# Performance work log

Measured on AMD Instinct MI355X. Metric: run time of the kernel, lower is better.

Reference implementation:

```python
import math
import jax, jax.numpy as jnp
import numpy as np

CAPACITY_FACTOR = 1.25
TOP_K = 2
LN_EPS = 1e-5


def setup_inputs() -> dict:
    key = jax.random.key(0)
    ks = jax.random.split(key, 4)
    B, S, D, F, E = 8, 4096, 256, 512, 8
    x = jax.random.normal(ks[0], (B, S, D), dtype=jnp.float32)
    Wr = jax.random.normal(ks[1], (D, E), dtype=jnp.float32) / np.sqrt(D)
    br = jnp.zeros((E,), jnp.float32)
    W1 = jax.random.normal(ks[2], (E, D, F), dtype=jnp.float32) / np.sqrt(D)
    b1 = jnp.zeros((E, F), jnp.float32)
    W2 = jax.random.normal(ks[3], (E, F, D), dtype=jnp.float32) / np.sqrt(F)
    b2 = jnp.zeros((E, D), jnp.float32)
    gamma = jnp.ones((D,), jnp.float32)
    beta = jnp.zeros((D,), jnp.float32)
    return {"x": x, "Wr": Wr, "br": br, "W1": W1, "b1": b1,
            "W2": W2, "b2": b2, "gamma": gamma, "beta": beta}


def _layer_norm(x, gamma, beta):
    mu = jnp.mean(x, axis=-1, keepdims=True)
    var = jnp.var(x, axis=-1, keepdims=True)
    return (x - mu) * jax.lax.rsqrt(var + LN_EPS) * gamma + beta


def reference(x, Wr, br, W1, b1, W2, b2, gamma, beta):
    B, S, D = x.shape
    E = Wr.shape[1]
    N = B * S
    K = TOP_K

    # --- Router: per-sequence softmax routing weights [B, E] ---
    logits = jnp.mean(x, axis=1) @ Wr + br              # [B, E]
    routing_weights = jax.nn.softmax(logits, axis=-1)   # [B, E]

    # --- Capacity constraints (SparseMoELayer._apply_capacity_constraints) ---
    capacity = float(math.ceil(N * CAPACITY_FACTOR / E))
    expected_loads = routing_weights.sum(axis=0) * (N / B)          # [E]
    scale = jnp.where(expected_loads > capacity,
                      capacity / expected_loads, 1.0)               # [E]
    routing_weights = jax.nn.softmax(routing_weights * scale, axis=-1)

    # --- Expand to tokens and take top-k, renormalize with softmax ---
    rw_tok = jnp.broadcast_to(routing_weights[:, None, :], (B, S, E)).reshape(N, E)
    top_w, top_i = jax.lax.top_k(rw_tok, K)             # [N, K]
    top_w = jax.nn.softmax(top_w, axis=-1)

    # --- Expert FFNs (dense compute over all experts, sparse combine) ---
    xf = x.reshape(N, D)
    h = jax.nn.gelu(jnp.einsum('nd,edf->enf', xf, W1) + b1[:, None, :],
                    approximate=False)                  # [E, N, F]
    y = jnp.einsum('enf,efd->end', h, W2) + b2[:, None, :]  # [E, N, D]

    # dense combine weights [N, E] via scatter-add of top-k weights
    w_dense = jnp.zeros((N, E), x.dtype).at[jnp.arange(N)[:, None], top_i].add(top_w)
    out = jnp.einsum('ne,end->nd', w_dense, y).reshape(B, S, D)

    # residual + layer norm
    out = _layer_norm(out + x, gamma, beta)
    return out
```

## Files before the change

### kernel.cpp

```cpp
#include <hip/hip_runtime.h>
#include <math.h>


#define B_ 8
#define S_ 4096
#define D_ 256
#define F_ 512
#define E_ 8

typedef short bf16x8 __attribute__((ext_vector_type(8)));
typedef float f32x4 __attribute__((ext_vector_type(4)));

static __device__ __forceinline__ unsigned short f2bf(float f) {
    union { float f; unsigned int i; } v; v.f = f;
    unsigned int x = v.i;
    return (unsigned short)((x + 0x7fffu + ((x >> 16) & 1u)) >> 16);
}

static __device__ __forceinline__ unsigned int cvt_pk_bf16(float s0, float s1) {
    unsigned int r;
    asm("v_cvt_pk_bf16_f32 %0, %1, %2" : "=v"(r) : "v"(s0), "v"(s1));
    return r;
}

static __device__ __forceinline__ void bar_lds() {
    asm volatile("s_waitcnt lgkmcnt(0)" ::: "memory");
    __builtin_amdgcn_s_barrier();
}

static __device__ __forceinline__ float gelu_f(float v) {
    float x = fabsf(v) * 0.70710678118654752f;
    float t = __builtin_amdgcn_rcpf(1.0f + 0.3275911f * x);
    float p = t * (0.254829592f +
              t * (-0.284496736f +
              t * (1.421413741f +
              t * (-1.453152027f +
              t * 1.061405429f))));
    float er = 1.0f - p * __expf(-x * x);
    er = __builtin_copysignf(er, v);
    return 0.5f * v * (1.0f + er);
}

__global__ void k_prep(const float* __restrict__ x,
                       double* __restrict__ partial,
                       const float* __restrict__ W1,
                       const float* __restrict__ W2,
                       unsigned short* __restrict__ W1T,
                       unsigned short* __restrict__ W2T) {
    int bid = blockIdx.x;
    if (bid < 512) {
        int b = bid >> 6;
        int c = bid & 63;
        int d = threadIdx.x;
        const float* p = x + ((size_t)(b * S_ + c * 64) * D_ + d);
        double acc = 0.0;
        #pragma unroll 8
        for (int i = 0; i < 64; ++i) acc += (double)p[(size_t)i * D_];
        partial[(size_t)bid * D_ + d] = acc;
        return;
    }
    __shared__ float tile[32][33];
    const float* src;
    unsigned short* dst;
    int R, C, cb, rb;
    if (bid < 1536) {
        int b2 = bid - 512;
        int e = b2 >> 7, rem = b2 & 127;
        int by = rem >> 4, bx = rem & 15;
        R = 256; C = 512;
        src = W1 + (size_t)e * R * C;
        dst = W1T + (size_t)e * R * C;
        cb = bx * 32; rb = by * 32;
    } else {
        int b2 = bid - 1536;
        int e = b2 >> 7, rem = b2 & 127;
        int by = rem >> 3, bx = rem & 7;
        R = 512; C = 256;
        src = W2 + (size_t)e * R * C;
        dst = W2T + (size_t)e * R * C;
        cb = bx * 32; rb = by * 32;
    }
    int tx = threadIdx.x & 31, ty = threadIdx.x >> 5;
    #pragma unroll
    for (int k = 0; k < 4; ++k)
        tile[ty + 8 * k][tx] = src[(size_t)(rb + ty + 8 * k) * C + cb + tx];
    __syncthreads();
    #pragma unroll
    for (int k = 0; k < 4; ++k)
        dst[(size_t)(cb + ty + 8 * k) * R + rb + tx] = f2bf(tile[tx][ty + 8 * k]);
}

__global__ void k_red2(const double* __restrict__ partial,
                       const float* __restrict__ Wr,
                       const float* __restrict__ br,
                       double* __restrict__ lgout) {
    __shared__ double xs[256];
    int bb = blockIdx.x;
    int t = threadIdx.x;
    double acc = 0.0;
    #pragma unroll 8
    for (int c = 0; c < 64; ++c)
        acc += partial[(size_t)(bb * 64 + c) * D_ + t];
    xs[t] = acc;
    __syncthreads();
    if (t < 8) {
        int e = t;
        double a2 = 0.0;
        for (int d = 0; d < D_; ++d)
            a2 += (xs[d] * (1.0 / (double)S_)) * (double)Wr[d * E_ + e];
        lgout[bb * 8 + e] = a2 + (double)br[e];
    }
}

__global__ void k_router(const double* __restrict__ lgin,
                         float* __restrict__ route) {
    __shared__ double lg[64];
    __shared__ double rw[8][8];
    int t = threadIdx.x;
    if (t < 64) lg[t] = lgin[t];
    __syncthreads();
    if (t < 8) {
        int bb = t;
        double m = -1e300;
        for (int ee = 0; ee < 8; ++ee) m = fmax(m, lg[bb * 8 + ee]);
        double s = 0.0;
        double p[8];
        for (int ee = 0; ee < 8; ++ee) { p[ee] = exp(lg[bb * 8 + ee] - m); s += p[ee]; }
        for (int ee = 0; ee < 8; ++ee) rw[bb][ee] = p[ee] / s;
    }
    __syncthreads();
    if (t < 8) {
        int bb = t;
        const double capacity = 5120.0;
        double scale[8];
        for (int ee = 0; ee < 8; ++ee) {
            double load = 0.0;
            for (int b2 = 0; b2 < 8; ++b2) load += rw[b2][ee];
            load *= 4096.0;
            scale[ee] = load > capacity ? capacity / load : 1.0;
        }
        double v[8];
        double m = -1e300;
        for (int ee = 0; ee < 8; ++ee) { v[ee] = rw[bb][ee] * scale[ee]; m = fmax(m, v[ee]); }
        double s = 0.0;
        for (int ee = 0; ee < 8; ++ee) { v[ee] = exp(v[ee] - m); s += v[ee]; }
        for (int ee = 0; ee < 8; ++ee) v[ee] /= s;
        int i1 = 0;
        for (int ee = 1; ee < 8; ++ee) if (v[ee] > v[i1]) i1 = ee;
        int i2 = (i1 == 0) ? 1 : 0;
        for (int ee = 0; ee < 8; ++ee) { if (ee == i1) continue; if (v[ee] > v[i2]) i2 = ee; }
        double d21 = v[i2] - v[i1];
        double ed = exp(d21);
        double w1 = 1.0 / (1.0 + ed);
        double w2 = ed * w1;
        route[bb * 4 + 0] = (float)i1;
        route[bb * 4 + 1] = (float)i2;
        route[bb * 4 + 2] = (float)w1;
        route[bb * 4 + 3] = (float)w2;
    }
}

__launch_bounds__(512, 4)
__global__ void k_moe_m(const float* __restrict__ xf,
                        const unsigned short* __restrict__ W1T,
                        const unsigned short* __restrict__ W2T,
                        const float* __restrict__ b1,
                        const float* __restrict__ b2,
                        const float* __restrict__ gamma,
                        const float* __restrict__ beta,
                        const float* __restrict__ route,
                        float* __restrict__ out) {
    __shared__ __align__(16) unsigned short Xsb[64][264];
    __shared__ __align__(16) unsigned short Hsb[2][64][136];
    __shared__ float gbuf[256], bbuf[256];
    __shared__ __align__(16) float rred[64][20];

    const int t = threadIdx.x;
    const int wv = t >> 6;
    const int lane = t & 63;
    const int g = lane >> 4;
    const int c = lane & 15;
    const int b = blockIdx.x & 7;
    const int m0 = (blockIdx.x >> 3) * 64;

    if (t < 256) { gbuf[t] = gamma[t]; bbuf[t] = beta[t]; }

    const int e0i = (int)route[b * 4 + 0];
    const int e1i = (int)route[b * 4 + 1];
    const float rw0 = route[b * 4 + 2];
    const float rw1 = route[b * 4 + 3];

    {
        int row = t >> 3;
        int col0 = (t & 7) * 32;
        const float* src = xf + ((size_t)(b * S_ + m0 + row) * D_ + col0);
        #pragma unroll
        for (int jg = 0; jg < 4; ++jg) {
            float4 a0 = *(const float4*)(src + jg * 8);
            float4 a1 = *(const float4*)(src + jg * 8 + 4);
            union { unsigned int pk[4]; uint4 q; } o;
            o.pk[0] = cvt_pk_bf16(a0.x, a0.y);
            o.pk[1] = cvt_pk_bf16(a0.z, a0.w);
            o.pk[2] = cvt_pk_bf16(a1.x, a1.y);
            o.pk[3] = cvt_pk_bf16(a1.z, a1.w);
            *(uint4*)&Xsb[row][col0 + jg * 8] = o.q;
        }
    }

    f32x4 Yacc[4][2];
    #pragma unroll
    for (int i = 0; i < 4; ++i)
        #pragma unroll
        for (int j = 0; j < 2; ++j)
            #pragma unroll
            for (int r = 0; r < 4; ++r) Yacc[i][j][r] = 0.f;

    bf16x8 w1f[8];
    {
        const unsigned short* w1p0 =
            W1T + ((size_t)(e0i * F_ + wv * 16 + c)) * D_ + g * 8;
        #pragma unroll
        for (int kc = 0; kc < 8; ++kc)
            w1f[kc] = *(const bf16x8*)(w1p0 + kc * 32);
    }

    bar_lds();

    int pb = 0;
    for (int it = 0; it < 8; ++it) {
        const int sl = it >> 2;
        const int fb = it & 3;
        const int e = sl ? e1i : e0i;
        const float w = sl ? rw1 : rw0;

        const unsigned short* w2p =
            W2T + ((size_t)(e * D_ + wv * 32 + c)) * F_ + fb * 128 + g * 8;
        bf16x8 w2f[4][2];
        #pragma unroll
        for (int kc = 0; kc < 4; ++kc)
            #pragma unroll
            for (int nt = 0; nt < 2; ++nt)
                w2f[kc][nt] = *(const bf16x8*)(w2p + (size_t)(nt * 16) * F_ + kc * 32);

        float4 bias4 = *(const float4*)&b1[e * F_ + fb * 128 + wv * 16 + g * 4];

        f32x4 Hacc[4];
        #pragma unroll
        for (int i = 0; i < 4; ++i)
            #pragma unroll
            for (int r = 0; r < 4; ++r) Hacc[i][r] = 0.f;
        #pragma unroll
        for (int kc = 0; kc < 8; ++kc) {
            #pragma unroll
            for (int mt = 0; mt < 4; ++mt) {
                bf16x8 a = *(const bf16x8*)&Xsb[mt * 16 + c][kc * 32 + g * 8];
                Hacc[mt] = __builtin_amdgcn_mfma_f32_16x16x32_bf16(w1f[kc], a, Hacc[mt], 0, 0, 0);
            }
        }

        #pragma unroll
        for (int mt = 0; mt < 4; ++mt) {
            float h0 = w * gelu_f(Hacc[mt][0] + bias4.x);
            float h1 = w * gelu_f(Hacc[mt][1] + bias4.y);
            float h2 = w * gelu_f(Hacc[mt][2] + bias4.z);
            float h3 = w * gelu_f(Hacc[mt][3] + bias4.w);
            uint2 q;
            q.x = cvt_pk_bf16(h0, h1);
            q.y = cvt_pk_bf16(h2, h3);
            *(uint2*)&Hsb[pb][mt * 16 + c][wv * 16 + g * 4] = q;
        }

        {
            const int itn = (it + 1) & 7;
            const int en = (itn >> 2) ? e1i : e0i;
            const int fbn = itn & 3;
            const unsigned short* w1pn =
                W1T + ((size_t)(en * F_ + fbn * 128 + wv * 16 + c)) * D_ + g * 8;
            #pragma unroll
            for (int kc = 0; kc < 8; ++kc)
                w1f[kc] = *(const bf16x8*)(w1pn + kc * 32);
        }

        bar_lds();

        #pragma unroll
        for (int kc = 0; kc < 4; ++kc) {
            #pragma unroll
            for (int mt = 0; mt < 4; ++mt) {
                bf16x8 a = *(const bf16x8*)&Hsb[pb][mt * 16 + c][kc * 32 + g * 8];
                #pragma unroll
                for (int nt = 0; nt < 2; ++nt)
                    Yacc[mt][nt] = __builtin_amdgcn_mfma_f32_16x16x32_bf16(a, w2f[kc][nt], Yacc[mt][nt], 0, 0, 0);
            }
        }
        pb ^= 1;
    }

    float bias2[2];
    #pragma unroll
    for (int nt = 0; nt < 2; ++nt) {
        int d = wv * 32 + nt * 16 + c;
        bias2[nt] = rw0 * b2[e0i * D_ + d] + rw1 * b2[e1i * D_ + d];
    }
    #pragma unroll
    for (int mt = 0; mt < 4; ++mt)
        #pragma unroll
        for (int r = 0; r < 4; ++r) {
            int row = mt * 16 + g * 4 + r;
            const float* xr = xf + (size_t)(b * S_ + m0 + row) * D_;
            float s = 0.f, sq = 0.f;
            #pragma unroll
            for (int nt = 0; nt < 2; ++nt) {
                int d = wv * 32 + nt * 16 + c;
                float v = Yacc[mt][nt][r] + bias2[nt] + xr[d];
                Yacc[mt][nt][r] = v;
                s += v; sq += v * v;
            }
            s += __shfl_xor(s, 1); sq += __shfl_xor(sq, 1);
            s += __shfl_xor(s, 2); sq += __shfl_xor(sq, 2);
            s += __shfl_xor(s, 4); sq += __shfl_xor(sq, 4);
            s += __shfl_xor(s, 8); sq += __shfl_xor(sq, 8);
            if (c == 0) { rred[row][wv * 2] = s; rred[row][wv * 2 + 1] = sq; }
        }
    bar_lds();
    #pragma unroll
    for (int mt = 0; mt < 4; ++mt)
        #pragma unroll
        for (int r = 0; r < 4; ++r) {
            int row = mt * 16 + g * 4 + r;
            float4 p0 = *(const float4*)&rred[row][0];
            float4 p1 = *(const float4*)&rred[row][4];
            float4 p2 = *(const float4*)&rred[row][8];
            float4 p3 = *(const float4*)&rred[row][12];
            float s  = ((p0.x + p1.x) + (p2.x + p3.x)) + ((p0.z + p1.z) + (p2.z + p3.z));
            float sq = ((p0.y + p1.y) + (p2.y + p3.y)) + ((p0.w + p1.w) + (p2.w + p3.w));
            float mu = s * (1.0f / 256.0f);
            float var = sq * (1.0f / 256.0f) - mu * mu;
            float rstd = rsqrtf(var + 1e-5f);
            float* op = out + (size_t)(b * S_ + m0 + row) * D_;
            #pragma unroll
            for (int nt = 0; nt < 2; ++nt) {
                int d = wv * 32 + nt * 16 + c;
                op[d] = (Yacc[mt][nt][r] - mu) * rstd * gbuf[d] + bbuf[d];
            }
        }
}

extern "C" void kernel_launch(void* const* d_in, const int* in_sizes, int n_in,
                              void* d_out, int out_size, void* d_ws, size_t ws_size,
                              hipStream_t stream) {
    const float* x     = (const float*)d_in[0];
    const float* Wr    = (const float*)d_in[1];
    const float* br    = (const float*)d_in[2];
    const float* W1    = (const float*)d_in[3];
    const float* b1    = (const float*)d_in[4];
    const float* W2    = (const float*)d_in[5];
    const float* b2    = (const float*)d_in[6];
    const float* gamma = (const float*)d_in[7];
    const float* beta  = (const float*)d_in[8];
    float* out = (float*)d_out;

    char* ws = (char*)d_ws;
    double* partial = (double*)ws;
    float* route  = (float*)(ws + 1064960);
    double* lg    = (double*)(ws + 1065472);
    unsigned short* W1T = (unsigned short*)(ws + 1081344);
    unsigned short* W2T = (unsigned short*)(ws + 3178496);

    hipLaunchKernelGGL(k_prep, dim3(2560), dim3(256), 0, stream,
                       x, partial, W1, W2, W1T, W2T);
    hipLaunchKernelGGL(k_red2, dim3(8), dim3(256), 0, stream,
                       partial, Wr, br, lg);
    hipLaunchKernelGGL(k_router, dim3(1), dim3(64), 0, stream,
                       lg, route);
    hipLaunchKernelGGL(k_moe_m, dim3(512), dim3(512), 0, stream,
                       x, W1T, W2T, b1, b2, gamma, beta, route, out);
}
```

Before: 201.9 us.

## Software-pipeline expert FFN loop so GEMM2 of previous block overlaps GELU

Restructures the 8-step expert loop into a prologue, a skewed steady state and an epilogue. Each iteration now computes GEMM1 for block it, then interleaves the GELU/pack of those results with the GEMM2 MFMAs of block it-1 read from the other LDS buffer. This leaves one barrier per iteration and overlaps transcendental VALU work with matrix work. The cost is a more complex control flow, a longer-lived w2f register set and possible register pressure.

```diff
diff --git a/kernel.cpp b/kernel.cpp
--- a/kernel.cpp
+++ b/kernel.cpp
@@ -226,24 +226,10 @@
 
     bar_lds();
 
-    int pb = 0;
-    for (int it = 0; it < 8; ++it) {
-        const int sl = it >> 2;
-        const int fb = it & 3;
-        const int e = sl ? e1i : e0i;
-        const float w = sl ? rw1 : rw0;
-
-        const unsigned short* w2p =
-            W2T + ((size_t)(e * D_ + wv * 32 + c)) * F_ + fb * 128 + g * 8;
-        bf16x8 w2f[4][2];
-        #pragma unroll
-        for (int kc = 0; kc < 4; ++kc)
-            #pragma unroll
-            for (int nt = 0; nt < 2; ++nt)
-                w2f[kc][nt] = *(const bf16x8*)(w2p + (size_t)(nt * 16) * F_ + kc * 32);
-
-        float4 bias4 = *(const float4*)&b1[e * F_ + fb * 128 + wv * 16 + g * 4];
-
+    bf16x8 w2f[4][2];
+
+    {
+        float4 bias4 = *(const float4*)&b1[e0i * F_ + wv * 16 + g * 4];
         f32x4 Hacc[4];
         #pragma unroll
         for (int i = 0; i < 4; ++i)
@@ -257,43 +243,109 @@
                 Hacc[mt] = __builtin_amdgcn_mfma_f32_16x16x32_bf16(w1f[kc], a, Hacc[mt], 0, 0, 0);
             }
         }
-
         #pragma unroll
         for (int mt = 0; mt < 4; ++mt) {
-            float h0 = w * gelu_f(Hacc[mt][0] + bias4.x);
-            float h1 = w * gelu_f(Hacc[mt][1] + bias4.y);
-            float h2 = w * gelu_f(Hacc[mt][2] + bias4.z);
-            float h3 = w * gelu_f(Hacc[mt][3] + bias4.w);
+            float h0 = rw0 * gelu_f(Hacc[mt][0] + bias4.x);
+            float h1 = rw0 * gelu_f(Hacc[mt][1] + bias4.y);
+            float h2 = rw0 * gelu_f(Hacc[mt][2] + bias4.z);
+            float h3 = rw0 * gelu_f(Hacc[mt][3] + bias4.w);
             uint2 q;
             q.x = cvt_pk_bf16(h0, h1);
             q.y = cvt_pk_bf16(h2, h3);
-            *(uint2*)&Hsb[pb][mt * 16 + c][wv * 16 + g * 4] = q;
-        }
-
-        {
-            const int itn = (it + 1) & 7;
-            const int en = (itn >> 2) ? e1i : e0i;
+            *(uint2*)&Hsb[0][mt * 16 + c][wv * 16 + g * 4] = q;
+        }
+        const unsigned short* w1pn =
+            W1T + ((size_t)(e0i * F_ + 128 + wv * 16 + c)) * D_ + g * 8;
+        #pragma unroll
+        for (int kc = 0; kc < 8; ++kc)
+            w1f[kc] = *(const bf16x8*)(w1pn + kc * 32);
+        bar_lds();
+    }
+
+    for (int it = 1; it < 8; ++it) {
+        const int e  = (it >= 4) ? e1i : e0i;
+        const float w = (it >= 4) ? rw1 : rw0;
+        const int fb = it & 3;
+        const int ep  = ((it - 1) >= 4) ? e1i : e0i;
+        const int fbp = (it - 1) & 3;
+        const int wb = it & 1;
+
+        const unsigned short* w2p =
+            W2T + ((size_t)(ep * D_ + wv * 32 + c)) * F_ + fbp * 128 + g * 8;
+        #pragma unroll
+        for (int kc = 0; kc < 4; ++kc)
+            #pragma unroll
+            for (int nt = 0; nt < 2; ++nt)
+                w2f[kc][nt] = *(const bf16x8*)(w2p + (size_t)(nt * 16) * F_ + kc * 32);
+
+        float4 bias4 = *(const float4*)&b1[e * F_ + fb * 128 + wv * 16 + g * 4];
+
+        f32x4 Hacc[4];
+        #pragma unroll
+        for (int i = 0; i < 4; ++i)
+            #pragma unroll
+            for (int r = 0; r < 4; ++r) Hacc[i][r] = 0.f;
+        #pragma unroll
+        for (int kc = 0; kc < 8; ++kc) {
+            #pragma unroll
+            for (int mt = 0; mt < 4; ++mt) {
+                bf16x8 a = *(const bf16x8*)&Xsb[mt * 16 + c][kc * 32 + g * 8];
+                Hacc[mt] = __builtin_amdgcn_mfma_f32_16x16x32_bf16(w1f[kc], a, Hacc[mt], 0, 0, 0);
+            }
+        }
+
+        #pragma unroll
+        for (int u = 0; u < 4; ++u) {
+            {
+                float h0 = w * gelu_f(Hacc[u][0] + bias4.x);
+                float h1 = w * gelu_f(Hacc[u][1] + bias4.y);
+                float h2 = w * gelu_f(Hacc[u][2] + bias4.z);
+                float h3 = w * gelu_f(Hacc[u][3] + bias4.w);
+                uint2 q;
+                q.x = cvt_pk_bf16(h0, h1);
+                q.y = cvt_pk_bf16(h2, h3);
+                *(uint2*)&Hsb[wb][u * 16 + c][wv * 16 + g * 4] = q;
+            }
+            #pragma unroll
+            for (int mt = 0; mt < 4; ++mt) {
+                bf16x8 a = *(const bf16x8*)&Hsb[wb ^ 1][mt * 16 + c][u * 32 + g * 8];
+                #pragma unroll
+                for (int nt = 0; nt < 2; ++nt)
+                    Yacc[mt][nt] = __builtin_amdgcn_mfma_f32_16x16x32_bf16(a, w2f[u][nt], Yacc[mt][nt], 0, 0, 0);
+            }
+        }
+
+        if (it < 7) {
+            const int itn = it + 1;
+            const int en = (itn >= 4) ? e1i : e0i;
             const int fbn = itn & 3;
             const unsigned short* w1pn =
                 W1T + ((size_t)(en * F_ + fbn * 128 + wv * 16 + c)) * D_ + g * 8;
             #pragma unroll
             for (int kc = 0; kc < 8; ++kc)
                 w1f[kc] = *(const bf16x8*)(w1pn + kc * 32);
-        }
-
-        bar_lds();
-
-        #pragma unroll
-        for (int kc = 0; kc < 4; ++kc) {
-            #pragma unroll
-            for (int mt = 0; mt < 4; ++mt) {
-                bf16x8 a = *(const bf16x8*)&Hsb[pb][mt * 16 + c][kc * 32 + g * 8];
+        } else {
+            const unsigned short* w2p7 =
+                W2T + ((size_t)(e1i * D_ + wv * 32 + c)) * F_ + 3 * 128 + g * 8;
+            #pragma unroll
+            for (int kc = 0; kc < 4; ++kc)
                 #pragma unroll
                 for (int nt = 0; nt < 2; ++nt)
-                    Yacc[mt][nt] = __builtin_amdgcn_mfma_f32_16x16x32_bf16(a, w2f[kc][nt], Yacc[mt][nt], 0, 0, 0);
-            }
-        }
-        pb ^= 1;
+                    w2f[kc][nt] = *(const bf16x8*)(w2p7 + (size_t)(nt * 16) * F_ + kc * 32);
+        }
+
+        bar_lds();
+    }
+
+    #pragma unroll
+    for (int kc = 0; kc < 4; ++kc) {
+        #pragma unroll
+        for (int mt = 0; mt < 4; ++mt) {
+            bf16x8 a = *(const bf16x8*)&Hsb[1][mt * 16 + c][kc * 32 + g * 8];
+            #pragma unroll
+            for (int nt = 0; nt < 2; ++nt)
+                Yacc[mt][nt] = __builtin_amdgcn_mfma_f32_16x16x32_bf16(a, w2f[kc][nt], Yacc[mt][nt], 0, 0, 0);
+        }
     }
 
     float bias2[2];
```

Measured after the change: 209.1 us. 3.5% more time.

## Switch expert FFN MFMAs to 32x32x16 tiles with 2x4 wave grid

Applied to the files above, without the earlier changes.

Replaces the 16x16x32 bf16 MFMA tiling with 32x32x16 MFMAs, reorganising the 8 waves into a 2 (rows) by 4 (F/D columns) grid so each wave owns a 32x32 H tile and a 32x64 output tile. W1 fragments are now loaded in two halves per iteration and W2 fragments partly streamed from global inside the second GEMM loop. The aim is fewer MFMA issues and fewer LDS reads per flop. In exchange the register footprint and global-load latency exposure change, and the per-wave LDS bank pattern is different.

```diff
diff --git a/kernel.cpp b/kernel.cpp
--- a/kernel.cpp
+++ b/kernel.cpp
@@ -10,6 +10,7 @@
 
 typedef short bf16x8 __attribute__((ext_vector_type(8)));
 typedef float f32x4 __attribute__((ext_vector_type(4)));
+typedef float f32x16 __attribute__((ext_vector_type(16)));
 
 static __device__ __forceinline__ unsigned short f2bf(float f) {
     union { float f; unsigned int i; } v; v.f = f;
@@ -173,13 +174,16 @@
     __shared__ __align__(16) unsigned short Xsb[64][264];
     __shared__ __align__(16) unsigned short Hsb[2][64][136];
     __shared__ float gbuf[256], bbuf[256];
-    __shared__ __align__(16) float rred[64][20];
+    __shared__ __align__(16) float rred[64][8];
 
     const int t = threadIdx.x;
     const int wv = t >> 6;
     const int lane = t & 63;
-    const int g = lane >> 4;
-    const int c = lane & 15;
+    const int lo = lane & 31;
+    const int hi = lane >> 5;
+    const int fi = wv & 3;
+    const int mi = wv >> 2;
+    const int di = wv & 3;
     const int b = blockIdx.x & 7;
     const int m0 = (blockIdx.x >> 3) * 64;
 
@@ -207,143 +211,138 @@
         }
     }
 
-    f32x4 Yacc[4][2];
-    #pragma unroll
-    for (int i = 0; i < 4; ++i)
-        #pragma unroll
-        for (int j = 0; j < 2; ++j)
-            #pragma unroll
-            for (int r = 0; r < 4; ++r) Yacc[i][j][r] = 0.f;
-
-    bf16x8 w1f[8];
+    f32x16 Yacc[2];
+    #pragma unroll
+    for (int j = 0; j < 2; ++j)
+        #pragma unroll
+        for (int r = 0; r < 16; ++r) Yacc[j][r] = 0.f;
+
+    bf16x8 w1h[8];
     {
         const unsigned short* w1p0 =
-            W1T + ((size_t)(e0i * F_ + wv * 16 + c)) * D_ + g * 8;
-        #pragma unroll
-        for (int kc = 0; kc < 8; ++kc)
-            w1f[kc] = *(const bf16x8*)(w1p0 + kc * 32);
+            W1T + ((size_t)(e0i * F_ + fi * 32 + lo)) * D_ + hi * 8;
+        #pragma unroll
+        for (int k = 0; k < 8; ++k)
+            w1h[k] = *(const bf16x8*)(w1p0 + k * 16);
     }
 
     bar_lds();
 
-    int pb = 0;
     for (int it = 0; it < 8; ++it) {
-        const int sl = it >> 2;
+        const int e  = (it >= 4) ? e1i : e0i;
+        const float w = (it >= 4) ? rw1 : rw0;
         const int fb = it & 3;
-        const int e = sl ? e1i : e0i;
-        const float w = sl ? rw1 : rw0;
-
-        const unsigned short* w2p =
-            W2T + ((size_t)(e * D_ + wv * 32 + c)) * F_ + fb * 128 + g * 8;
-        bf16x8 w2f[4][2];
-        #pragma unroll
-        for (int kc = 0; kc < 4; ++kc)
-            #pragma unroll
-            for (int nt = 0; nt < 2; ++nt)
-                w2f[kc][nt] = *(const bf16x8*)(w2p + (size_t)(nt * 16) * F_ + kc * 32);
-
-        float4 bias4 = *(const float4*)&b1[e * F_ + fb * 128 + wv * 16 + g * 4];
-
-        f32x4 Hacc[4];
-        #pragma unroll
-        for (int i = 0; i < 4; ++i)
-            #pragma unroll
-            for (int r = 0; r < 4; ++r) Hacc[i][r] = 0.f;
-        #pragma unroll
-        for (int kc = 0; kc < 8; ++kc) {
-            #pragma unroll
-            for (int mt = 0; mt < 4; ++mt) {
-                bf16x8 a = *(const bf16x8*)&Xsb[mt * 16 + c][kc * 32 + g * 8];
-                Hacc[mt] = __builtin_amdgcn_mfma_f32_16x16x32_bf16(w1f[kc], a, Hacc[mt], 0, 0, 0);
-            }
-        }
-
-        #pragma unroll
-        for (int mt = 0; mt < 4; ++mt) {
-            float h0 = w * gelu_f(Hacc[mt][0] + bias4.x);
-            float h1 = w * gelu_f(Hacc[mt][1] + bias4.y);
-            float h2 = w * gelu_f(Hacc[mt][2] + bias4.z);
-            float h3 = w * gelu_f(Hacc[mt][3] + bias4.w);
+        const int wb = it & 1;
+
+        const unsigned short* w1p =
+            W1T + ((size_t)(e * F_ + fb * 128 + fi * 32 + lo)) * D_ + hi * 8;
+
+        f32x16 Hacc;
+        #pragma unroll
+        for (int r = 0; r < 16; ++r) Hacc[r] = 0.f;
+        #pragma unroll
+        for (int k = 0; k < 8; ++k) {
+            bf16x8 xa = *(const bf16x8*)&Xsb[mi * 32 + lo][k * 16 + hi * 8];
+            Hacc = __builtin_amdgcn_mfma_f32_32x32x16_bf16(w1h[k], xa, Hacc, 0, 0, 0);
+        }
+        #pragma unroll
+        for (int k = 0; k < 8; ++k)
+            w1h[k] = *(const bf16x8*)(w1p + (8 + k) * 16);
+        #pragma unroll
+        for (int k = 0; k < 8; ++k) {
+            bf16x8 xa = *(const bf16x8*)&Xsb[mi * 32 + lo][(8 + k) * 16 + hi * 8];
+            Hacc = __builtin_amdgcn_mfma_f32_32x32x16_bf16(w1h[k], xa, Hacc, 0, 0, 0);
+        }
+
+        #pragma unroll
+        for (int q4 = 0; q4 < 4; ++q4) {
+            int f0 = 8 * q4 + 4 * hi;
+            float4 bb4 = *(const float4*)&b1[e * F_ + fb * 128 + fi * 32 + f0];
+            float h0 = w * gelu_f(Hacc[q4 * 4 + 0] + bb4.x);
+            float h1 = w * gelu_f(Hacc[q4 * 4 + 1] + bb4.y);
+            float h2 = w * gelu_f(Hacc[q4 * 4 + 2] + bb4.z);
+            float h3 = w * gelu_f(Hacc[q4 * 4 + 3] + bb4.w);
             uint2 q;
             q.x = cvt_pk_bf16(h0, h1);
             q.y = cvt_pk_bf16(h2, h3);
-            *(uint2*)&Hsb[pb][mt * 16 + c][wv * 16 + g * 4] = q;
+            *(uint2*)&Hsb[wb][mi * 32 + lo][fi * 32 + f0] = q;
+        }
+
+        const unsigned short* w2p =
+            W2T + ((size_t)(e * D_ + di * 64 + lo)) * F_ + fb * 128 + hi * 8;
+        bf16x8 w2a0 = *(const bf16x8*)(w2p);
+        bf16x8 w2b0 = *(const bf16x8*)(w2p + (size_t)32 * F_);
+        bf16x8 w2a1 = *(const bf16x8*)(w2p + 16);
+        bf16x8 w2b1 = *(const bf16x8*)(w2p + (size_t)32 * F_ + 16);
+
+        bar_lds();
+
+        #pragma unroll
+        for (int kc = 0; kc < 8; ++kc) {
+            bf16x8 ha = *(const bf16x8*)&Hsb[wb][mi * 32 + lo][kc * 16 + hi * 8];
+            bf16x8 wa = (kc == 0) ? w2a0 : (kc == 1) ? w2a1
+                        : *(const bf16x8*)(w2p + kc * 16);
+            bf16x8 wbv = (kc == 0) ? w2b0 : (kc == 1) ? w2b1
+                        : *(const bf16x8*)(w2p + (size_t)32 * F_ + kc * 16);
+            Yacc[0] = __builtin_amdgcn_mfma_f32_32x32x16_bf16(ha, wa, Yacc[0], 0, 0, 0);
+            Yacc[1] = __builtin_amdgcn_mfma_f32_32x32x16_bf16(ha, wbv, Yacc[1], 0, 0, 0);
         }
 
         {
             const int itn = (it + 1) & 7;
-            const int en = (itn >> 2) ? e1i : e0i;
+            const int en = (itn >= 4) ? e1i : e0i;
             const int fbn = itn & 3;
             const unsigned short* w1pn =
-                W1T + ((size_t)(en * F_ + fbn * 128 + wv * 16 + c)) * D_ + g * 8;
+                W1T + ((size_t)(en * F_ + fbn * 128 + fi * 32 + lo)) * D_ + hi * 8;
             #pragma unroll
-            for (int kc = 0; kc < 8; ++kc)
-                w1f[kc] = *(const bf16x8*)(w1pn + kc * 32);
-        }
-
-        bar_lds();
-
-        #pragma unroll
-        for (int kc = 0; kc < 4; ++kc) {
-            #pragma unroll
-            for (int mt = 0; mt < 4; ++mt) {
-                bf16x8 a = *(const bf16x8*)&Hsb[pb][mt * 16 + c][kc * 32 + g * 8];
-                #pragma unroll
-                for (int nt = 0; nt < 2; ++nt)
-                    Yacc[mt][nt] = __builtin_amdgcn_mfma_f32_16x16x32_bf16(a, w2f[kc][nt], Yacc[mt][nt], 0, 0, 0);
-            }
-        }
-        pb ^= 1;
-    }
-
-    float bias2[2];
-    #pragma unroll
-    for (int nt = 0; nt < 2; ++nt) {
-        int d = wv * 32 + nt * 16 + c;
-        bias2[nt] = rw0 * b2[e0i * D_ + d] + rw1 * b2[e1i * D_ + d];
-    }
-    #pragma unroll
-    for (int mt = 0; mt < 4; ++mt)
-        #pragma unroll
-        for (int r = 0; r < 4; ++r) {
-            int row = mt * 16 + g * 4 + r;
-            const float* xr = xf + (size_t)(b * S_ + m0 + row) * D_;
-            float s = 0.f, sq = 0.f;
-            #pragma unroll
-            for (int nt = 0; nt < 2; ++nt) {
-                int d = wv * 32 + nt * 16 + c;
-                float v = Yacc[mt][nt][r] + bias2[nt] + xr[d];
-                Yacc[mt][nt][r] = v;
-                s += v; sq += v * v;
-            }
-            s += __shfl_xor(s, 1); sq += __shfl_xor(sq, 1);
-            s += __shfl_xor(s, 2); sq += __shfl_xor(sq, 2);
-            s += __shfl_xor(s, 4); sq += __shfl_xor(sq, 4);
-            s += __shfl_xor(s, 8); sq += __shfl_xor(sq, 8);
-            if (c == 0) { rred[row][wv * 2] = s; rred[row][wv * 2 + 1] = sq; }
-        }
+            for (int k = 0; k < 8; ++k)
+                w1h[k] = *(const bf16x8*)(w1pn + k * 16);
+        }
+    }
+
+    float bias2v[2];
+    #pragma unroll
+    for (int dt = 0; dt < 2; ++dt) {
+        int d = di * 64 + dt * 32 + lo;
+        bias2v[dt] = rw0 * b2[e0i * D_ + d] + rw1 * b2[e1i * D_ + d];
+    }
+    #pragma unroll
+    for (int r = 0; r < 16; ++r) {
+        int row = mi * 32 + (r & 3) + 8 * (r >> 2) + 4 * hi;
+        const float* xr = xf + (size_t)(b * S_ + m0 + row) * D_;
+        float s = 0.f, sq = 0.f;
+        #pragma unroll
+        for (int dt = 0; dt < 2; ++dt) {
+            int d = di * 64 + dt * 32 + lo;
+            float v = Yacc[dt][r] + bias2v[dt] + xr[d];
+            Yacc[dt][r] = v;
+            s += v; sq += v * v;
+        }
+        s += __shfl_xor(s, 1);  sq += __shfl_xor(sq, 1);
+        s += __shfl_xor(s, 2);  sq += __shfl_xor(sq, 2);
+        s += __shfl_xor(s, 4);  sq += __shfl_xor(sq, 4);
+        s += __shfl_xor(s, 8);  sq += __shfl_xor(sq, 8);
+        s += __shfl_xor(s, 16); sq += __shfl_xor(sq, 16);
+        if (lo == 0) { rred[row][di * 2] = s; rred[row][di * 2 + 1] = sq; }
+    }
     bar_lds();
     #pragma unroll
-    for (int mt = 0; mt < 4; ++mt)
-        #pragma unroll
-        for (int r = 0; r < 4; ++r) {
-            int row = mt * 16 + g * 4 + r;
-            float4 p0 = *(const float4*)&rred[row][0];
-            float4 p1 = *(const float4*)&rred[row][4];
-            float4 p2 = *(const float4*)&rred[row][8];
-            float4 p3 = *(const float4*)&rred[row][12];
-            float s  = ((p0.x + p1.x) + (p2.x + p3.x)) + ((p0.z + p1.z) + (p2.z + p3.z));
-            float sq = ((p0.y + p1.y) + (p2.y + p3.y)) + ((p0.w + p1.w) + (p2.w + p3.w));
-            float mu = s * (1.0f / 256.0f);
-            float var = sq * (1.0f / 256.0f) - mu * mu;
-            float rstd = rsqrtf(var + 1e-5f);
-            float* op = out + (size_t)(b * S_ + m0 + row) * D_;
-            #pragma unroll
-            for (int nt = 0; nt < 2; ++nt) {
-                int d = wv * 32 + nt * 16 + c;
-                op[d] = (Yacc[mt][nt][r] - mu) * rstd * gbuf[d] + bbuf[d];
-            }
-        }
+    for (int r = 0; r < 16; ++r) {
+        int row = mi * 32 + (r & 3) + 8 * (r >> 2) + 4 * hi;
+        float4 p0 = *(const float4*)&rred[row][0];
+        float4 p1 = *(const float4*)&rred[row][4];
+        float s  = (p0.x + p0.z) + (p1.x + p1.z);
+        float sq = (p0.y + p0.w) + (p1.y + p1.w);
+        float mu = s * (1.0f / 256.0f);
+        float var = sq * (1.0f / 256.0f) - mu * mu;
+        float rstd = rsqrtf(var + 1e-5f);
+        float* op = out + (size_t)(b * S_ + m0 + row) * D_;
+        #pragma unroll
+        for (int dt = 0; dt < 2; ++dt) {
+            int d = di * 64 + dt * 32 + lo;
+            op[d] = (Yacc[dt][r] - mu) * rstd * gbuf[d] + bbuf[d];
+        }
+    }
 }
 
 extern "C" void kernel_launch(void* const* d_in, const int* in_sizes, int n_in,
```

Measured after the change: 261.1 us. 1.29x slower.
